# Kernel tuning notes

Hardware: AMD Instinct MI355X
Metric: run time of the kernel (lower is better)

The kernel has to match this reference:

```python
import jax, jax.numpy as jnp
import numpy as np

B, N, D = 4, 2048, 1024
H, HD = 16, 64
S = 11  # n_scales
D4 = jnp.array([0.4829629131445341, 0.8365163037378079,
                0.2241438680420134, -0.1294095225512604], dtype=jnp.float32)


def _causal_dilated_d4(f, d):
    """Causal depthwise D4 conv with dilation d along axis 2. f: [B,H,N,HD].
    Matches torch F.pad(x,(3d,0)) + F.conv1d(dilation=d, groups=C):
    y[n] = sum_t D4[t] * f[n - (3-t)*d]."""
    n = f.shape[2]
    fp = jnp.pad(f, ((0, 0), (0, 0), (3 * d, 0), (0, 0)))
    return (D4[0] * fp[:, :, 0:n, :]
            + D4[1] * fp[:, :, d:d + n, :]
            + D4[2] * fp[:, :, 2 * d:2 * d + n, :]
            + D4[3] * fp[:, :, 3 * d:3 * d + n, :])


def setup_inputs() -> dict:
    key = jax.random.key(0)
    ks = jax.random.split(key, 10)
    s = 0.02
    return {
        "x": jax.random.normal(ks[0], (B, N, D), dtype=jnp.float32),
        "Wqkv": jax.random.normal(ks[1], (3 * D, D), dtype=jnp.float32) * s,
        "bqkv": jnp.zeros((3 * D,), dtype=jnp.float32),
        "Wo": jax.random.normal(ks[2], (D, D), dtype=jnp.float32) * s,
        "bo": jnp.zeros((D,), dtype=jnp.float32),
        "Wg": jax.random.normal(ks[3], (D, D), dtype=jnp.float32) * s,
        "bg": jnp.full((D,), 2.0, dtype=jnp.float32),
        "scale_gain": jnp.zeros((S, H), dtype=jnp.float32),
        "Wqs": jax.random.normal(ks[4], (S, HD), dtype=jnp.float32) * 0.01,
        "field_coupling": jnp.eye(H, dtype=jnp.float32)
        + 0.01 * jax.random.normal(ks[5], (H, H), dtype=jnp.float32),
    }


def reference(x, Wqkv, bqkv, Wo, bo, Wg, bg, scale_gain, Wqs, field_coupling):
    b, n, d = x.shape
    qkv = x @ Wqkv.T + bqkv                          # [B,N,3D]
    q, k, v = jnp.split(qkv, 3, axis=-1)
    q = q.reshape(b, n, H, HD).transpose(0, 2, 1, 3)  # [B,H,N,HD]
    k = k.reshape(b, n, H, HD).transpose(0, 2, 1, 3)
    v = v.reshape(b, n, H, HD).transpose(0, 2, 1, 3)

    # per-position scale gains: learned prior + query-conditioned offset
    q_offset = jnp.einsum('bhnd,sd->bhns', q, Wqs)    # [B,H,N,S]
    prior = scale_gain.T[None, :, None, :]            # [1,H,1,S]
    gains = jax.nn.softmax(q_offset + prior, axis=-1)

    # deposit: field[i] = V[i] * ||K[i]||
    k_mag = jnp.linalg.norm(k, axis=-1, keepdims=True)
    field = v * k_mag                                 # [B,H,N,HD]

    # propagate: causal multiscale dilated D4 conv, gain-weighted accumulate
    out_field = jnp.zeros_like(field)
    for j in range(S):
        y = _causal_dilated_d4(field, 1 << j)
        out_field = out_field + gains[:, :, :, j:j + 1] * y

    coupling = jax.nn.softmax(field_coupling, axis=-1)
    out_field = jnp.einsum('ij,bjnd->bind', coupling, out_field)

    gate = jax.nn.sigmoid(x @ Wg.T + bg)              # [B,N,D]
    gathered = out_field.transpose(0, 2, 1, 3).reshape(b, n, d)
    return (gathered * gate) @ Wo.T + bo
```

## Files before the change

### kernel.cpp

```cpp
#include <hip/hip_runtime.h>
#include <hip/hip_bf16.h>
#include <stdint.h>
#include <math.h>

#define BB 4
#define NN 2048
#define DD 1024
#define HH 16
#define HDD 64
#define SS 11

#define D4_0 0.4829629131445341f
#define D4_1 0.8365163037378079f
#define D4_2 0.2241438680420134f
#define D4_3 (-0.1294095225512604f)

typedef __bf16 bf16_t;
typedef __bf16 bf16x4_t __attribute__((ext_vector_type(4)));
typedef __bf16 bf16x8_t __attribute__((ext_vector_type(8)));
typedef float f32x4_t __attribute__((ext_vector_type(4)));

__global__ __launch_bounds__(256) void cvt_all_k(const float* __restrict__ s0,
                                                 const float* __restrict__ s1,
                                                 const float* __restrict__ s2,
                                                 const float* __restrict__ s3,
                                                 bf16_t* __restrict__ d0,
                                                 bf16_t* __restrict__ d1,
                                                 bf16_t* __restrict__ d2,
                                                 bf16_t* __restrict__ d3) {
  const int n0 = 2097152, n1 = 786432, n2 = 262144, n3 = 262144;
  int i = blockIdx.x * 256 + threadIdx.x;
  const float* s;
  bf16_t* d;
  if (i < n0) { s = s0; d = d0; }
  else if (i < n0 + n1) { i -= n0; s = s1; d = d1; }
  else if (i < n0 + n1 + n2) { i -= n0 + n1; s = s2; d = d2; }
  else { i -= n0 + n1 + n2; if (i >= n3) return; s = s3; d = d3; }
  f32x4_t v = ((const f32x4_t*)s)[i];
  bf16x4_t o;
  o[0] = (bf16_t)v[0]; o[1] = (bf16_t)v[1]; o[2] = (bf16_t)v[2]; o[3] = (bf16_t)v[3];
  ((bf16x4_t*)d)[i] = o;
}

__device__ __forceinline__ void gload16(const void* g, void* l) {
  __builtin_amdgcn_global_load_lds((__attribute__((address_space(1))) void*)(void*)g,
                                   (__attribute__((address_space(3))) void*)l,
                                   16, 0, 0);
}

__global__ __launch_bounds__(512, 2) void gemm256(const bf16_t* __restrict__ Aa,
                                                  const bf16_t* __restrict__ Bw,
                                                  const float* __restrict__ bias0,
                                                  const float* __restrict__ bias1,
                                                  bf16_t* __restrict__ out0,
                                                  bf16_t* __restrict__ out1) {
  __shared__ bf16_t sA[2][16384];
  __shared__ bf16_t sB[2][16384];

  const int tid = threadIdx.x;
  const int s = (blockIdx.x & 7) * 64 + (blockIdx.x >> 3);
  const int mtile = s >> 4;
  const int ntile = s & 15;
  const int row0 = mtile << 8;
  const int col0 = ntile << 8;

  const int w = tid >> 6, lane = tid & 63;
  const int wm = w >> 2, wn = w & 3;
  const int wmbase = wm << 7;
  const int wnbase = wn << 6;
  const int m16 = lane & 15, quad = lane >> 4;

  f32x4_t acc[8][4];
#pragma unroll
  for (int i = 0; i < 8; i++)
#pragma unroll
    for (int jq = 0; jq < 4; jq++) acc[i][jq] = (f32x4_t){0.f, 0.f, 0.f, 0.f};

  auto stage_half = [&](int buf, int tensor, int half, int t) {
    if (t >= 16) return;
    const bf16_t* gb = tensor ? Bw : Aa;
    const int gr0 = (tensor ? col0 : row0) + (half << 7);
    const int kb = t << 6;
    bf16_t* lbase = (tensor ? sB[buf] : sA[buf]) + (half << 13);
#pragma unroll
    for (int l = 0; l < 2; ++l) {
      int c = l * 512 + tid;
      int row = c >> 3, kc = c & 7;
      int swz = kc ^ (row & 7);
      const bf16_t* g = gb + (size_t)(gr0 + row) * 1024 + kb + swz * 8;
      bf16_t* lp = lbase + ((l * 512 + (tid & 448)) << 3);
      gload16(g, lp);
    }
  };

  bf16x8_t af[4], bfr[4];
  auto rdA = [&](int buf, int ih, int ks) {
#pragma unroll
    for (int i = 0; i < 4; i++) {
      int ar = wmbase + ((ih * 4 + i) << 4) + m16;
      int kc = (ks << 2) + quad;
      af[i] = *(const bf16x8_t*)&sA[buf][ar * 64 + ((kc ^ (ar & 7)) << 3)];
    }
  };
  auto rdB = [&](int buf, int ks) {
#pragma unroll
    for (int jq = 0; jq < 4; jq++) {
      int br = wnbase + (jq << 4) + m16;
      int kc = (ks << 2) + quad;
      bfr[jq] = *(const bf16x8_t*)&sB[buf][br * 64 + ((kc ^ (br & 7)) << 3)];
    }
  };
  auto domfma = [&](int ih) {
#pragma unroll
    for (int i = 0; i < 4; i++)
#pragma unroll
      for (int jq = 0; jq < 4; jq++)
        acc[ih * 4 + i][jq] =
            __builtin_amdgcn_mfma_f32_16x16x32_bf16(af[i], bfr[jq], acc[ih * 4 + i][jq], 0, 0, 0);
  };

#define PH_ENTER()                                        \
  __builtin_amdgcn_s_barrier();                           \
  asm volatile("s_waitcnt lgkmcnt(0)" ::: "memory");      \
  __builtin_amdgcn_sched_barrier(0);                      \
  __builtin_amdgcn_s_setprio(1)
#define PH_EXIT()                                         \
  __builtin_amdgcn_s_setprio(0);                          \
  __builtin_amdgcn_s_barrier()
#define PH_EXIT_V4()                                      \
  __builtin_amdgcn_s_setprio(0);                          \
  asm volatile("s_waitcnt vmcnt(4)" ::: "memory");        \
  __builtin_amdgcn_s_barrier()
#define PH_EXIT_V0()                                      \
  __builtin_amdgcn_s_setprio(0);                          \
  asm volatile("s_waitcnt vmcnt(0)" ::: "memory");        \
  __builtin_amdgcn_s_barrier()

  stage_half(0, 0, 0, 0); stage_half(0, 0, 1, 0);
  stage_half(0, 1, 0, 0); stage_half(0, 1, 1, 0);
  stage_half(1, 1, 0, 1); stage_half(1, 1, 1, 1);
  asm volatile("s_waitcnt vmcnt(4)" ::: "memory");
  __builtin_amdgcn_s_barrier();

  for (int it = 0; it < 8; ++it) {
    const int Tb = 2 * it + 1, T2 = 2 * it + 2, T3 = 2 * it + 3;
    rdA(0, 0, 0); rdB(0, 0);
    stage_half(1, 0, 0, Tb); stage_half(1, 0, 1, Tb);
    PH_ENTER(); domfma(0); PH_EXIT();
    rdA(0, 1, 0);
    PH_ENTER(); domfma(1); PH_EXIT();
    rdA(0, 0, 1); rdB(0, 1);
    PH_ENTER(); domfma(0); PH_EXIT();
    rdA(0, 1, 1);
    stage_half(0, 1, 0, T2); stage_half(0, 1, 1, T2);
    PH_ENTER(); domfma(1);
    if (T2 < 16) { PH_EXIT_V4(); } else { PH_EXIT_V0(); }
    rdA(1, 0, 0); rdB(1, 0);
    stage_half(0, 0, 0, T2); stage_half(0, 0, 1, T2);
    PH_ENTER(); domfma(0); PH_EXIT();
    rdA(1, 1, 0);
    PH_ENTER(); domfma(1); PH_EXIT();
    rdA(1, 0, 1); rdB(1, 1);
    PH_ENTER(); domfma(0); PH_EXIT();
    rdA(1, 1, 1);
    stage_half(1, 1, 0, T3); stage_half(1, 1, 1, T3);
    PH_ENTER(); domfma(1);
    if (T3 < 16) { PH_EXIT_V4(); } else { PH_EXIT_V0(); }
  }
#undef PH_ENTER
#undef PH_EXIT
#undef PH_EXIT_V4
#undef PH_EXIT_V0

  const bool is_gate = (col0 >= 3072);
#pragma unroll
  for (int i = 0; i < 8; i++) {
#pragma unroll
    for (int jq = 0; jq < 4; jq++) {
      const int grow0 = row0 + wmbase + (i << 4) + (quad << 2);
      const int gcol = col0 + wnbase + (jq << 4) + m16;
      const float bval = is_gate ? bias1[gcol - 3072] : bias0[gcol];
#pragma unroll
      for (int r = 0; r < 4; r++) {
        float val = acc[i][jq][r] + bval;
        if (is_gate)
          out1[(size_t)(grow0 + r) * 1024 + (gcol - 3072)] =
              (bf16_t)(1.f / (1.f + __expf(-val)));
        else
          out0[(size_t)(grow0 + r) * 3072 + gcol] = (bf16_t)val;
      }
    }
  }
}

template <int MODE>
__global__ __launch_bounds__(256) void gemm_nt(const bf16_t* __restrict__ A,
                                               const bf16_t* __restrict__ Bw,
                                               const float* __restrict__ bias0,
                                               const float* __restrict__ bias1,
                                               void* __restrict__ out0v,
                                               void* __restrict__ out1v,
                                               int M, int Nn, int K) {
  __shared__ bf16_t As[128 * 64];
  __shared__ bf16_t Bs[128 * 64];

  const int tid = threadIdx.x;
  const int ntiles = Nn >> 7;
  const int grp = ntiles << 3;
  const int g = blockIdx.x / grp;
  const int j = blockIdx.x % grp;
  const int mtile = (g << 3) | (j & 7);
  const int ntile = j >> 3;
  const int row0 = mtile << 7;
  const int col0 = ntile << 7;
  const int w = tid >> 6, lane = tid & 63;
  const int wm = w >> 1, wn = w & 1;
  const int m16 = lane & 15, quad = lane >> 4;

  f32x4_t acc[4][4];
#pragma unroll
  for (int i = 0; i < 4; i++)
#pragma unroll
    for (int jj = 0; jj < 4; jj++) acc[i][jj] = (f32x4_t){0.f, 0.f, 0.f, 0.f};

  for (int kb = 0; kb < K; kb += 64) {
    __syncthreads();
#pragma unroll
    for (int r = 0; r < 4; ++r) {
      int c = r * 256 + tid;
      int row = c >> 3, kc = c & 7;
      int swz = kc ^ (row & 7);
      const bf16_t* gpA = A + (size_t)(row0 + row) * K + kb + swz * 8;
      const bf16_t* gpB = Bw + (size_t)(col0 + row) * K + kb + swz * 8;
      bf16_t* lpA = As + (size_t)(r * 256 + (tid & 192)) * 8;
      bf16_t* lpB = Bs + (size_t)(r * 256 + (tid & 192)) * 8;
      gload16(gpA, lpA);
      gload16(gpB, lpB);
    }
    __syncthreads();

#pragma unroll
    for (int kk = 0; kk < 2; ++kk) {
      bf16x8_t af[4], bfr[4];
      const int kc = (kk << 2) + quad;
#pragma unroll
      for (int i = 0; i < 4; i++) {
        int arow = (wm << 6) + (i << 4) + m16;
        af[i] = *(const bf16x8_t*)(As + arow * 64 + ((kc ^ (arow & 7)) << 3));
        int brow = (wn << 6) + (i << 4) + m16;
        bfr[i] = *(const bf16x8_t*)(Bs + brow * 64 + ((kc ^ (brow & 7)) << 3));
      }
#pragma unroll
      for (int i = 0; i < 4; i++)
#pragma unroll
        for (int jj = 0; jj < 4; jj++)
          acc[i][jj] = __builtin_amdgcn_mfma_f32_16x16x32_bf16(af[i], bfr[jj], acc[i][jj], 0, 0, 0);
    }
  }

#pragma unroll
  for (int i = 0; i < 4; i++) {
#pragma unroll
    for (int jj = 0; jj < 4; jj++) {
      const int grow0 = row0 + (wm << 6) + (i << 4) + (quad << 2);
      const int gcol = col0 + (wn << 6) + (jj << 4) + m16;
      const float bval = (MODE == 0)
                             ? (gcol < 3072 ? bias0[gcol] : bias1[gcol - 3072])
                             : bias0[gcol];
#pragma unroll
      for (int r = 0; r < 4; r++) {
        float val = acc[i][jj][r] + bval;
        if (MODE == 0) {
          if (gcol < 3072)
            ((bf16_t*)out0v)[(size_t)(grow0 + r) * 3072 + gcol] = (bf16_t)val;
          else
            ((bf16_t*)out1v)[(size_t)(grow0 + r) * 1024 + (gcol - 3072)] =
                (bf16_t)(1.f / (1.f + __expf(-val)));
        } else {
          ((float*)out0v)[(size_t)(grow0 + r) * Nn + gcol] = val;
        }
      }
    }
  }
}

__global__ __launch_bounds__(256) void field_gains_k(const bf16_t* __restrict__ qkvb,
                                                     const float* __restrict__ scale_gain,
                                                     const float* __restrict__ Wqs,
                                                     bf16_t* __restrict__ fieldb,
                                                     float* __restrict__ gains) {
  __shared__ float skmag[4 * 16];
  const int tid = threadIdx.x;
  const int w = tid >> 6, lane = tid & 63;
  const int bn = blockIdx.x * 4 + w;
  const int b = bn >> 11, n_pos = bn & 2047;
  const int m16 = lane & 15, quad = lane >> 4;
  const bf16_t* qp = qkvb + (size_t)bn * 3072;

  bf16x8_t aq[2], ak[2], bw[2];
#pragma unroll
  for (int it = 0; it < 2; it++) {
    const int koff = it * 32 + quad * 8;
    aq[it] = *(const bf16x8_t*)(qp + m16 * 64 + koff);
    ak[it] = *(const bf16x8_t*)(qp + 1024 + m16 * 64 + koff);
    bf16x8_t bwv;
    if (m16 < SS) {
      const float* wp = Wqs + m16 * 64 + koff;
#pragma unroll
      for (int j = 0; j < 8; j++) bwv[j] = (bf16_t)wp[j];
    } else {
#pragma unroll
      for (int j = 0; j < 8; j++) bwv[j] = (bf16_t)0.f;
    }
    bw[it] = bwv;
  }

  f32x4_t acc_l = (f32x4_t){0.f, 0.f, 0.f, 0.f};
  f32x4_t acc_k = (f32x4_t){0.f, 0.f, 0.f, 0.f};
#pragma unroll
  for (int it = 0; it < 2; it++) {
    acc_l = __builtin_amdgcn_mfma_f32_16x16x32_bf16(aq[it], bw[it], acc_l, 0, 0, 0);
    acc_k = __builtin_amdgcn_mfma_f32_16x16x32_bf16(ak[it], ak[it], acc_k, 0, 0, 0);
  }

#pragma unroll
  for (int r = 0; r < 4; r++) {
    if (m16 == quad * 4 + r) skmag[w * 16 + m16] = sqrtf(fmaxf(acc_k[r], 0.f));
  }

#pragma unroll
  for (int r = 0; r < 4; r++) {
    const int m = quad * 4 + r;
    float lg = (m16 < SS) ? (acc_l[r] + scale_gain[m16 * 16 + m]) : -1e30f;
    float mx = lg;
#pragma unroll
    for (int sh = 1; sh < 16; sh <<= 1) mx = fmaxf(mx, __shfl_xor(mx, sh, 64));
    float e = (m16 < SS) ? __expf(lg - mx) : 0.f;
    float se = e;
#pragma unroll
    for (int sh = 1; sh < 16; sh <<= 1) se += __shfl_xor(se, sh, 64);
    if (m16 < SS)
      gains[((size_t)(b * 16 + m) * 2048 + n_pos) * SS + m16] = e / se;
  }

  __syncthreads();

  {
    const int h = lane >> 2;
    const int hd0 = (lane & 3) << 4;
    const float km = skmag[w * 16 + h];
    const bf16_t* vp = qp + 2048 + h * 64 + hd0;
    bf16x8_t v0 = *(const bf16x8_t*)vp;
    bf16x8_t v1 = *(const bf16x8_t*)(vp + 8);
    bf16x8_t o0, o1;
#pragma unroll
    for (int q = 0; q < 8; q++) {
      o0[q] = (bf16_t)((float)v0[q] * km);
      o1[q] = (bf16_t)((float)v1[q] * km);
    }
    bf16_t* fp = fieldb + (((size_t)(b * 16 + h)) * 2048 + n_pos) * 64 + hd0;
    *(bf16x8_t*)fp = o0;
    *(bf16x8_t*)(fp + 8) = o1;
  }
}

__global__ __launch_bounds__(1024) void conv_couple_k(const bf16_t* __restrict__ field,
                                                      const float* __restrict__ gains,
                                                      const float* __restrict__ fcoup,
                                                      const bf16_t* __restrict__ gate,
                                                      bf16_t* __restrict__ gmat) {
  __shared__ bf16_t fld[16 * 16 * 64];
  __shared__ float sgn[16 * 16 * SS];
  __shared__ float scn[256];
  const int tid = threadIdx.x;
  const int blk = blockIdx.x;
  const int b = blk >> 7;
  const int nt = blk & 127;
  const int n0 = nt * 16;

  if (tid < 16) {
    float row[16];
    float mx = -1e30f;
#pragma unroll
    for (int j = 0; j < 16; j++) { row[j] = fcoup[tid * 16 + j]; mx = fmaxf(mx, row[j]); }
    float se = 0.f;
#pragma unroll
    for (int j = 0; j < 16; j++) { row[j] = __expf(row[j] - mx); se += row[j]; }
    float inv = 1.f / se;
#pragma unroll
    for (int j = 0; j < 16; j++) scn[tid * 16 + j] = row[j] * inv;
  }

  for (int i = tid; i < 16 * 16 * SS; i += 1024) {
    const int hh = i / (16 * SS);
    const int rem = i - hh * (16 * SS);
    sgn[i] = gains[((size_t)(b * 16 + hh) * 2048 + n0) * SS + rem];
  }
  __syncthreads();

  const int w = tid >> 6, lane = tid & 63;
  const int nsub = lane >> 3, c = lane & 7;
  const bf16_t* frow = field + ((size_t)(b * 16 + w)) * 2048 * 64;

#pragma unroll
  for (int p = 0; p < 2; ++p) {
    const int nl = p * 8 + nsub;
    const int n = n0 + nl;
    float g[SS];
#pragma unroll
    for (int s = 0; s < SS; s++) g[s] = sgn[w * (16 * SS) + nl * SS + s];

    float acc[8];
    {
      bf16x8_t f0 = *(const bf16x8_t*)(frow + (size_t)n * 64 + c * 8);
#pragma unroll
      for (int q = 0; q < 8; q++) acc[q] = D4_3 * (float)f0[q];
    }
#pragma unroll
    for (int j = 0; j < 11; j++) {
      float wgt = D4_2 * g[j];
      if (j >= 1) wgt += D4_1 * g[j - 1];
      int rr = n - (1 << j);
      float wv = rr >= 0 ? wgt : 0.f;
      rr = rr >= 0 ? rr : 0;
      bf16x8_t fv = *(const bf16x8_t*)(frow + (size_t)rr * 64 + c * 8);
#pragma unroll
      for (int q = 0; q < 8; q++) acc[q] += wv * (float)fv[q];
    }
#pragma unroll
    for (int j = 0; j < 10; j++) {
      int rr = n - (3 << j);
      float wv = rr >= 0 ? (D4_0 * g[j]) : 0.f;
      rr = rr >= 0 ? rr : 0;
      bf16x8_t fv = *(const bf16x8_t*)(frow + (size_t)rr * 64 + c * 8);
#pragma unroll
      for (int q = 0; q < 8; q++) acc[q] += wv * (float)fv[q];
    }
    bf16x8_t o;
#pragma unroll
    for (int q = 0; q < 8; q++) o[q] = (bf16_t)acc[q];
    *(bf16x8_t*)&fld[w * 1024 + nl * 64 + c * 8] = o;
  }

  __syncthreads();

#pragma unroll
  for (int p = 0; p < 2; ++p) {
    const int nl = p * 8 + nsub;
    const int n = n0 + nl;
    float s8[8];
#pragma unroll
    for (int q = 0; q < 8; q++) s8[q] = 0.f;
#pragma unroll
    for (int j = 0; j < 16; j++) {
      const float cw = scn[w * 16 + j];
      bf16x8_t v = *(const bf16x8_t*)&fld[j * 1024 + nl * 64 + c * 8];
#pragma unroll
      for (int q = 0; q < 8; q++) s8[q] += cw * (float)v[q];
    }
    const size_t base = ((size_t)(b * 2048 + n)) * 1024 + w * 64 + c * 8;
    bf16x8_t gt = *(const bf16x8_t*)(gate + base);
    bf16x8_t o;
#pragma unroll
    for (int q = 0; q < 8; q++) o[q] = (bf16_t)(s8[q] * (float)gt[q]);
    *(bf16x8_t*)(gmat + base) = o;
  }
}

extern "C" void kernel_launch(void* const* d_in, const int* in_sizes, int n_in,
                              void* d_out, int out_size, void* d_ws, size_t ws_size,
                              hipStream_t stream) {
  (void)in_sizes; (void)n_in; (void)out_size; (void)ws_size;
  const float* x = (const float*)d_in[0];
  const float* Wqkv = (const float*)d_in[1];
  const float* bqkv = (const float*)d_in[2];
  const float* Wo = (const float*)d_in[3];
  const float* bo = (const float*)d_in[4];
  const float* Wg = (const float*)d_in[5];
  const float* bg = (const float*)d_in[6];
  const float* scale_gain = (const float*)d_in[7];
  const float* Wqs = (const float*)d_in[8];
  const float* fcoup = (const float*)d_in[9];

  char* ws = (char*)d_ws;
  size_t off = 0;
  auto alloc = [&](size_t bytes) {
    void* p = ws + off;
    off += (bytes + 255) & ~(size_t)255;
    return p;
  };
  bf16_t* xb = (bf16_t*)alloc(8192ull * 1024 * 2);
  bf16_t* Wab = (bf16_t*)alloc(4096ull * 1024 * 2);
  bf16_t* Wob = (bf16_t*)alloc(1024ull * 1024 * 2);
  bf16_t* qkvb = (bf16_t*)alloc(8192ull * 3072 * 2);
  bf16_t* gateb = (bf16_t*)alloc(8192ull * 1024 * 2);
  bf16_t* fieldb = (bf16_t*)alloc(8388608ull * 2);
  float* gains = (float*)alloc(8192ull * 16 * SS * 4);
  bf16_t* gmat = (bf16_t*)alloc(8192ull * 1024 * 2);

  cvt_all_k<<<13316, 256, 0, stream>>>(x, Wqkv, Wg, Wo,
                                       xb, Wab, Wab + 3072ull * 1024, Wob);

  gemm256<<<512, 512, 0, stream>>>(xb, Wab, bqkv, bg, qkvb, gateb);

  field_gains_k<<<2048, 256, 0, stream>>>(qkvb, scale_gain, Wqs, fieldb, gains);

  conv_couple_k<<<512, 1024, 0, stream>>>(fieldb, gains, fcoup, gateb, gmat);

  gemm_nt<1><<<64 * 8, 256, 0, stream>>>(gmat, Wob, bo, nullptr, (void*)d_out, nullptr, 8192, 1024, 1024);
}
```

Before: 269.7 us.

## Simplify GEMM pipeline to whole-tile double buffering with fewer barriers

Replaces the staggered half-tile prefetch schedule (A and B halves staged at different phases with vmcnt(4) waits) with a plain double buffer that stages a whole K-tile at once and waits with vmcnt(0) before switching buffers. It also merges pairs of MFMA phases so two domfma calls share one barrier/priority region, cutting barrier count roughly in half. This lowers sync overhead but shortens the lead time of global prefetches, which risks exposing memory latency. Registers and LDS use stay the same.

```diff
diff --git a/kernel.cpp b/kernel.cpp
--- a/kernel.cpp
+++ b/kernel.cpp
@@ -92,6 +92,10 @@
       gload16(g, lp);
     }
   };
+  auto stage_tile = [&](int buf, int t) {
+    stage_half(buf, 0, 0, t); stage_half(buf, 0, 1, t);
+    stage_half(buf, 1, 0, t); stage_half(buf, 1, 1, t);
+  };
 
   bf16x8_t af[4], bfr[4];
   auto rdA = [&](int buf, int ih, int ks) {
@@ -119,58 +123,54 @@
             __builtin_amdgcn_mfma_f32_16x16x32_bf16(af[i], bfr[jq], acc[ih * 4 + i][jq], 0, 0, 0);
   };
 
-#define PH_ENTER()                                        \
-  __builtin_amdgcn_s_barrier();                           \
-  asm volatile("s_waitcnt lgkmcnt(0)" ::: "memory");      \
-  __builtin_amdgcn_sched_barrier(0);                      \
-  __builtin_amdgcn_s_setprio(1)
-#define PH_EXIT()                                         \
-  __builtin_amdgcn_s_setprio(0);                          \
-  __builtin_amdgcn_s_barrier()
-#define PH_EXIT_V4()                                      \
-  __builtin_amdgcn_s_setprio(0);                          \
-  asm volatile("s_waitcnt vmcnt(4)" ::: "memory");        \
-  __builtin_amdgcn_s_barrier()
-#define PH_EXIT_V0()                                      \
-  __builtin_amdgcn_s_setprio(0);                          \
-  asm volatile("s_waitcnt vmcnt(0)" ::: "memory");        \
-  __builtin_amdgcn_s_barrier()
-
-  stage_half(0, 0, 0, 0); stage_half(0, 0, 1, 0);
-  stage_half(0, 1, 0, 0); stage_half(0, 1, 1, 0);
-  stage_half(1, 1, 0, 1); stage_half(1, 1, 1, 1);
-  asm volatile("s_waitcnt vmcnt(4)" ::: "memory");
-  __builtin_amdgcn_s_barrier();
+#define BAR() __builtin_amdgcn_s_barrier()
+#define WAITL0() asm volatile("s_waitcnt lgkmcnt(0)" ::: "memory"); __builtin_amdgcn_sched_barrier(0)
+#define PRIO1() __builtin_amdgcn_s_setprio(1)
+#define PRIO0() __builtin_amdgcn_s_setprio(0)
+#define WAITV0() asm volatile("s_waitcnt vmcnt(0)" ::: "memory")
+
+  stage_tile(0, 0);
+  WAITV0();
+  BAR();
 
   for (int it = 0; it < 8; ++it) {
-    const int Tb = 2 * it + 1, T2 = 2 * it + 2, T3 = 2 * it + 3;
+    const int O = 2 * it + 1, E2 = 2 * it + 2;
     rdA(0, 0, 0); rdB(0, 0);
-    stage_half(1, 0, 0, Tb); stage_half(1, 0, 1, Tb);
-    PH_ENTER(); domfma(0); PH_EXIT();
+    stage_tile(1, O);
+    BAR(); WAITL0(); PRIO1();
+    domfma(0);
     rdA(0, 1, 0);
-    PH_ENTER(); domfma(1); PH_EXIT();
+    WAITL0();
+    domfma(1);
+    PRIO0(); BAR();
     rdA(0, 0, 1); rdB(0, 1);
-    PH_ENTER(); domfma(0); PH_EXIT();
+    BAR(); WAITL0(); PRIO1();
+    domfma(0);
     rdA(0, 1, 1);
-    stage_half(0, 1, 0, T2); stage_half(0, 1, 1, T2);
-    PH_ENTER(); domfma(1);
-    if (T2 < 16) { PH_EXIT_V4(); } else { PH_EXIT_V0(); }
+    WAITL0();
+    domfma(1);
+    PRIO0(); WAITV0(); BAR();
     rdA(1, 0, 0); rdB(1, 0);
-    stage_half(0, 0, 0, T2); stage_half(0, 0, 1, T2);
-    PH_ENTER(); domfma(0); PH_EXIT();
+    stage_tile(0, E2);
+    BAR(); WAITL0(); PRIO1();
+    domfma(0);
     rdA(1, 1, 0);
-    PH_ENTER(); domfma(1); PH_EXIT();
+    WAITL0();
+    domfma(1);
+    PRIO0(); BAR();
     rdA(1, 0, 1); rdB(1, 1);
-    PH_ENTER(); domfma(0); PH_EXIT();
+    BAR(); WAITL0(); PRIO1();
+    domfma(0);
     rdA(1, 1, 1);
-    stage_half(1, 1, 0, T3); stage_half(1, 1, 1, T3);
-    PH_ENTER(); domfma(1);
-    if (T3 < 16) { PH_EXIT_V4(); } else { PH_EXIT_V0(); }
-  }
-#undef PH_ENTER
-#undef PH_EXIT
-#undef PH_EXIT_V4
-#undef PH_EXIT_V0
+    WAITL0();
+    domfma(1);
+    PRIO0(); WAITV0(); BAR();
+  }
+#undef BAR
+#undef WAITL0
+#undef PRIO1
+#undef PRIO0
+#undef WAITV0
 
   const bool is_gate = (col0 >= 3072);
 #pragma unroll
```

After: 266.5 us. No clear change (-1.2%).

## Fold Wqs into Wqkv so the GEMM produces query scale offsets directly

Applied to the files above, without the earlier changes.

Q is only used to compute the per-scale offsets q·Wqs, so a new kernel precomputes an effective weight matrix (Wq_h^T Wqs, 176 columns padded to 256) plus its bias. The main GEMM then computes K, V, gate and these 256 offset columns instead of the full 1024 Q columns, cutting its N from 4096 to 3328 and dropping the Q write. field_gains_k reads the precomputed fp32 offsets instead of running its own MFMA. It adds a small weight-preprocessing kernel each call and changes rounding, since the combined weight is cast to bf16.

```diff
diff --git a/kernel.cpp b/kernel.cpp
--- a/kernel.cpp
+++ b/kernel.cpp
@@ -28,7 +28,7 @@
                                                  bf16_t* __restrict__ d1,
                                                  bf16_t* __restrict__ d2,
                                                  bf16_t* __restrict__ d3) {
-  const int n0 = 2097152, n1 = 786432, n2 = 262144, n3 = 262144;
+  const int n0 = 2097152, n1 = 524288, n2 = 262144, n3 = 262144;
   int i = blockIdx.x * 256 + threadIdx.x;
   const float* s;
   bf16_t* d;
@@ -42,6 +42,40 @@
   ((bf16x4_t*)d)[i] = o;
 }
 
+__global__ __launch_bounds__(256) void weff_k(const float* __restrict__ Wqkv,
+                                              const float* __restrict__ Wqs,
+                                              const float* __restrict__ bqkv,
+                                              bf16_t* __restrict__ weff_out,
+                                              float* __restrict__ qbias) {
+  const int c = blockIdx.x;
+  const int t = threadIdx.x;
+  __shared__ float ws[64];
+  const int h = c / 11, sIdx = c - h * 11;
+  const bool valid = (c < 176);
+  if (t < 64) ws[t] = valid ? Wqs[sIdx * 64 + t] : 0.f;
+  __syncthreads();
+  f32x4_t acc = (f32x4_t){0.f, 0.f, 0.f, 0.f};
+  if (valid) {
+    const float* base = Wqkv + (size_t)(h * 64) * 1024 + t * 4;
+    for (int hd = 0; hd < 64; ++hd) {
+      f32x4_t v = *(const f32x4_t*)(base + (size_t)hd * 1024);
+      const float wv = ws[hd];
+      acc[0] += wv * v[0]; acc[1] += wv * v[1];
+      acc[2] += wv * v[2]; acc[3] += wv * v[3];
+    }
+  }
+  bf16x4_t o;
+  o[0] = (bf16_t)acc[0]; o[1] = (bf16_t)acc[1];
+  o[2] = (bf16_t)acc[2]; o[3] = (bf16_t)acc[3];
+  ((bf16x4_t*)(weff_out + (size_t)c * 1024))[t] = o;
+  if (t == 0) {
+    float b = 0.f;
+    if (valid)
+      for (int hd = 0; hd < 64; ++hd) b += bqkv[h * 64 + hd] * ws[hd];
+    qbias[c] = b;
+  }
+}
+
 __device__ __forceinline__ void gload16(const void* g, void* l) {
   __builtin_amdgcn_global_load_lds((__attribute__((address_space(1))) void*)(void*)g,
                                    (__attribute__((address_space(3))) void*)l,
@@ -50,17 +84,19 @@
 
 __global__ __launch_bounds__(512, 2) void gemm256(const bf16_t* __restrict__ Aa,
                                                   const bf16_t* __restrict__ Bw,
-                                                  const float* __restrict__ bias0,
-                                                  const float* __restrict__ bias1,
-                                                  bf16_t* __restrict__ out0,
-                                                  bf16_t* __restrict__ out1) {
+                                                  const float* __restrict__ bias_kv,
+                                                  const float* __restrict__ bias_g,
+                                                  const float* __restrict__ bias_q,
+                                                  bf16_t* __restrict__ kvb,
+                                                  bf16_t* __restrict__ gateb,
+                                                  float* __restrict__ qoffb) {
   __shared__ bf16_t sA[2][16384];
   __shared__ bf16_t sB[2][16384];
 
   const int tid = threadIdx.x;
-  const int s = (blockIdx.x & 7) * 64 + (blockIdx.x >> 3);
-  const int mtile = s >> 4;
-  const int ntile = s & 15;
+  const int s = (blockIdx.x & 7) * 52 + (blockIdx.x >> 3);
+  const int mtile = s / 13;
+  const int ntile = s - mtile * 13;
   const int row0 = mtile << 8;
   const int col0 = ntile << 8;
 
@@ -172,22 +208,26 @@
 #undef PH_EXIT_V4
 #undef PH_EXIT_V0
 
-  const bool is_gate = (col0 >= 3072);
+  const int kind = (ntile < 8) ? 0 : (ntile < 12 ? 1 : 2);
 #pragma unroll
   for (int i = 0; i < 8; i++) {
 #pragma unroll
     for (int jq = 0; jq < 4; jq++) {
       const int grow0 = row0 + wmbase + (i << 4) + (quad << 2);
       const int gcol = col0 + wnbase + (jq << 4) + m16;
-      const float bval = is_gate ? bias1[gcol - 3072] : bias0[gcol];
+      const float bval = (kind == 0) ? bias_kv[gcol]
+                       : (kind == 1) ? bias_g[gcol - 2048]
+                                     : bias_q[gcol - 3072];
 #pragma unroll
       for (int r = 0; r < 4; r++) {
         float val = acc[i][jq][r] + bval;
-        if (is_gate)
-          out1[(size_t)(grow0 + r) * 1024 + (gcol - 3072)] =
+        if (kind == 0)
+          kvb[(size_t)(grow0 + r) * 2048 + gcol] = (bf16_t)val;
+        else if (kind == 1)
+          gateb[(size_t)(grow0 + r) * 1024 + (gcol - 2048)] =
               (bf16_t)(1.f / (1.f + __expf(-val)));
         else
-          out0[(size_t)(grow0 + r) * 3072 + gcol] = (bf16_t)val;
+          qoffb[(size_t)(grow0 + r) * 256 + (gcol - 3072)] = val;
       }
     }
   }
@@ -264,29 +304,20 @@
     for (int jj = 0; jj < 4; jj++) {
       const int grow0 = row0 + (wm << 6) + (i << 4) + (quad << 2);
       const int gcol = col0 + (wn << 6) + (jj << 4) + m16;
-      const float bval = (MODE == 0)
-                             ? (gcol < 3072 ? bias0[gcol] : bias1[gcol - 3072])
-                             : bias0[gcol];
+      const float bval = bias0[gcol];
 #pragma unroll
       for (int r = 0; r < 4; r++) {
         float val = acc[i][jj][r] + bval;
-        if (MODE == 0) {
-          if (gcol < 3072)
-            ((bf16_t*)out0v)[(size_t)(grow0 + r) * 3072 + gcol] = (bf16_t)val;
-          else
-            ((bf16_t*)out1v)[(size_t)(grow0 + r) * 1024 + (gcol - 3072)] =
-                (bf16_t)(1.f / (1.f + __expf(-val)));
-        } else {
-          ((float*)out0v)[(size_t)(grow0 + r) * Nn + gcol] = val;
-        }
+        ((float*)out0v)[(size_t)(grow0 + r) * Nn + gcol] = val;
       }
     }
   }
-}
-
-__global__ __launch_bounds__(256) void field_gains_k(const bf16_t* __restrict__ qkvb,
+  (void)bias1; (void)out1v;
+}
+
+__global__ __launch_bounds__(256) void field_gains_k(const bf16_t* __restrict__ kvb,
+                                                     const float* __restrict__ qoffb,
                                                      const float* __restrict__ scale_gain,
-                                                     const float* __restrict__ Wqs,
                                                      bf16_t* __restrict__ fieldb,
                                                      float* __restrict__ gains) {
   __shared__ float skmag[4 * 16];
@@ -295,33 +326,19 @@
   const int bn = blockIdx.x * 4 + w;
   const int b = bn >> 11, n_pos = bn & 2047;
   const int m16 = lane & 15, quad = lane >> 4;
-  const bf16_t* qp = qkvb + (size_t)bn * 3072;
-
-  bf16x8_t aq[2], ak[2], bw[2];
+  const bf16_t* kp = kvb + (size_t)bn * 2048;
+
+  bf16x8_t ak[2];
 #pragma unroll
   for (int it = 0; it < 2; it++) {
     const int koff = it * 32 + quad * 8;
-    aq[it] = *(const bf16x8_t*)(qp + m16 * 64 + koff);
-    ak[it] = *(const bf16x8_t*)(qp + 1024 + m16 * 64 + koff);
-    bf16x8_t bwv;
-    if (m16 < SS) {
-      const float* wp = Wqs + m16 * 64 + koff;
-#pragma unroll
-      for (int j = 0; j < 8; j++) bwv[j] = (bf16_t)wp[j];
-    } else {
-#pragma unroll
-      for (int j = 0; j < 8; j++) bwv[j] = (bf16_t)0.f;
-    }
-    bw[it] = bwv;
-  }
-
-  f32x4_t acc_l = (f32x4_t){0.f, 0.f, 0.f, 0.f};
+    ak[it] = *(const bf16x8_t*)(kp + m16 * 64 + koff);
+  }
+
   f32x4_t acc_k = (f32x4_t){0.f, 0.f, 0.f, 0.f};
 #pragma unroll
-  for (int it = 0; it < 2; it++) {
-    acc_l = __builtin_amdgcn_mfma_f32_16x16x32_bf16(aq[it], bw[it], acc_l, 0, 0, 0);
+  for (int it = 0; it < 2; it++)
     acc_k = __builtin_amdgcn_mfma_f32_16x16x32_bf16(ak[it], ak[it], acc_k, 0, 0, 0);
-  }
 
 #pragma unroll
   for (int r = 0; r < 4; r++) {
@@ -331,7 +348,9 @@
 #pragma unroll
   for (int r = 0; r < 4; r++) {
     const int m = quad * 4 + r;
-    float lg = (m16 < SS) ? (acc_l[r] + scale_gain[m16 * 16 + m]) : -1e30f;
+    float lg = (m16 < SS)
+                   ? (qoffb[(size_t)bn * 256 + m * 11 + m16] + scale_gain[m16 * 16 + m])
+                   : -1e30f;
     float mx = lg;
 #pragma unroll
     for (int sh = 1; sh < 16; sh <<= 1) mx = fmaxf(mx, __shfl_xor(mx, sh, 64));
@@ -349,7 +368,7 @@
     const int h = lane >> 2;
     const int hd0 = (lane & 3) << 4;
     const float km = skmag[w * 16 + h];
-    const bf16_t* vp = qp + 2048 + h * 64 + hd0;
+    const bf16_t* vp = kp + 1024 + h * 64 + hd0;
     bf16x8_t v0 = *(const bf16x8_t*)vp;
     bf16x8_t v1 = *(const bf16x8_t*)(vp + 8);
     bf16x8_t o0, o1;
@@ -490,20 +509,24 @@
     return p;
   };
   bf16_t* xb = (bf16_t*)alloc(8192ull * 1024 * 2);
-  bf16_t* Wab = (bf16_t*)alloc(4096ull * 1024 * 2);
+  bf16_t* Wab = (bf16_t*)alloc(3328ull * 1024 * 2);
   bf16_t* Wob = (bf16_t*)alloc(1024ull * 1024 * 2);
-  bf16_t* qkvb = (bf16_t*)alloc(8192ull * 3072 * 2);
+  float* qbias = (float*)alloc(256 * 4);
+  bf16_t* kvb = (bf16_t*)alloc(8192ull * 2048 * 2);
   bf16_t* gateb = (bf16_t*)alloc(8192ull * 1024 * 2);
+  float* qoffb = (float*)alloc(8192ull * 256 * 4);
   bf16_t* fieldb = (bf16_t*)alloc(8388608ull * 2);
   float* gains = (float*)alloc(8192ull * 16 * SS * 4);
   bf16_t* gmat = (bf16_t*)alloc(8192ull * 1024 * 2);
 
-  cvt_all_k<<<13316, 256, 0, stream>>>(x, Wqkv, Wg, Wo,
-                                       xb, Wab, Wab + 3072ull * 1024, Wob);
-
-  gemm256<<<512, 512, 0, stream>>>(xb, Wab, bqkv, bg, qkvb, gateb);
-
-  field_gains_k<<<2048, 256, 0, stream>>>(qkvb, scale_gain, Wqs, fieldb, gains);
+  cvt_all_k<<<12288, 256, 0, stream>>>(x, Wqkv + 1024ull * 1024, Wg, Wo,
+                                       xb, Wab, Wab + 2048ull * 1024, Wob);
+
+  weff_k<<<256, 256, 0, stream>>>(Wqkv, Wqs, bqkv, Wab + 3072ull * 1024, qbias);
+
+  gemm256<<<416, 512, 0, stream>>>(xb, Wab, bqkv + 1024, bg, qbias, kvb, gateb, qoffb);
+
+  field_gains_k<<<2048, 256, 0, stream>>>(kvb, qoffb, scale_gain, fieldb, gains);
 
   conv_couple_k<<<512, 1024, 0, stream>>>(fieldb, gains, fcoup, gateb, gmat);
 
```

New measurement: 273.3 us. Within noise of the previous version (+1.3%).
